# Performance work log

Hardware: AMD Instinct MI355X
Metric: run time of the kernel (lower is better)

## Reference

```python
import jax, jax.numpy as jnp
import numpy as np

N, T, DM = 8192, 32, 128   # nodes, patches, d_model (d_in = T*DM = 4096)
M, NNZ = 1024, 131072      # hyperedges, incidences
EPS = 1e-5
SLOPE = 0.2


def _bn(x, g, b, axes):
    # BatchNorm with batch statistics (training-mode math, eval dropout)
    m = jnp.mean(x, axis=axes, keepdims=True)
    v = jnp.var(x, axis=axes, keepdims=True)
    return (x - m) / jnp.sqrt(v + EPS) * g + b


def _hconv(x, he_attr, he_n, he_e, W, att, bias, heads):
    # PyG HypergraphConv, use_attention=True, attention_mode='node', concat=False
    out = W.shape[1] // heads
    xt = (x @ W).reshape(N, heads, out)          # [N, H, F]
    et = (he_attr @ W).reshape(M, heads, out)    # [M, H, F]
    xi = xt[he_n]                                # [nnz, H, F] gather node feats
    ej = et[he_e]                                # [nnz, H, F] gather edge feats
    alpha = jnp.sum(jnp.concatenate([xi, ej], axis=-1) * att, axis=-1)  # [nnz, H]
    alpha = jax.nn.leaky_relu(alpha, SLOPE)
    # segment softmax grouped by hyperedge (attention_mode='node')
    amax = jax.ops.segment_max(alpha, he_e, num_segments=M)
    ex = jnp.exp(alpha - amax[he_e])
    alpha = ex / jax.ops.segment_sum(ex, he_e, num_segments=M)[he_e]
    # degree normalizers (hyperedge_weight == 1)
    ones = jnp.ones((NNZ,), x.dtype)
    Dn = jax.ops.segment_sum(ones, he_n, num_segments=N)
    Dinv = jnp.where(Dn > 0, 1.0 / Dn, 0.0)
    Bm = jax.ops.segment_sum(ones, he_e, num_segments=M)
    Binv = jnp.where(Bm > 0, 1.0 / Bm, 0.0)
    # node -> edge, then edge -> node message passing
    eo = jax.ops.segment_sum(alpha[:, :, None] * Binv[he_e][:, None, None] * xi,
                             he_e, num_segments=M)                     # [M, H, F]
    no = jax.ops.segment_sum(alpha[:, :, None] * Dinv[he_n][:, None, None] * eo[he_e],
                             he_n, num_segments=N)                     # [N, H, F]
    return no.mean(axis=1) + bias  # concat=False -> mean over heads


def setup_inputs() -> dict:
    key = jax.random.key(0)
    ks = jax.random.split(key, 16)
    d_in = T * DM
    s = 0.02
    inp = {
        "x": jax.random.normal(ks[0], (N, T, DM), jnp.float32),
        "he_nodes": jax.random.randint(ks[1], (NNZ,), 0, N),
        "he_edges": jax.random.randint(ks[2], (NNZ,), 0, M),
        "W1": jax.random.normal(ks[3], (d_in, DM), jnp.float32) * s,
        "b1": jnp.zeros((DM,), jnp.float32),
        "g1": jnp.ones((DM,), jnp.float32), "be1": jnp.zeros((DM,), jnp.float32),
        "Wh1": jax.random.normal(ks[4], (DM, 4 * DM), jnp.float32) * s,
        "att1": jax.random.normal(ks[5], (1, 4, 2 * DM), jnp.float32) * s,
        "bh1": jnp.zeros((DM,), jnp.float32),
        "g2": jnp.ones((DM,), jnp.float32), "be2": jnp.zeros((DM,), jnp.float32),
        "Wh2": jax.random.normal(ks[6], (DM, DM), jnp.float32) * s,
        "att2": jax.random.normal(ks[7], (1, 1, 2 * DM), jnp.float32) * s,
        "bh2": jnp.zeros((DM,), jnp.float32),
        "g3": jnp.ones((DM,), jnp.float32), "be3": jnp.zeros((DM,), jnp.float32),
        "W3": jax.random.normal(ks[8], (DM, d_in), jnp.float32) * s,
        "b3": jnp.zeros((d_in,), jnp.float32),
        "g4": jnp.ones((DM,), jnp.float32), "be4": jnp.zeros((DM,), jnp.float32),
    }
    return inp


def reference(x, he_nodes, he_edges, W1, b1, g1, be1, Wh1, att1, bh1,
              g2, be2, Wh2, att2, bh2, g3, be3, W3, b3, g4, be4):
    src = x
    h = x.reshape(N, T * DM)
    h = jax.nn.leaky_relu(h @ W1 + b1, SLOPE)
    h = _bn(h, g1, be1, 0)
    # hyperedge_attr = incidence^T @ h  (== to_dense_adj(...).T @ h)
    he_attr = jax.ops.segment_sum(h[he_nodes], he_edges, num_segments=M)
    h = h + _hconv(h, he_attr, he_nodes, he_edges, Wh1, att1, bh1, 4)
    h = _bn(h, g2, be2, 0)
    he_attr = jax.ops.segment_sum(h[he_nodes], he_edges, num_segments=M)
    h = h + _hconv(h, he_attr, he_nodes, he_edges, Wh2, att2, bh2, 1)
    h = _bn(h, g3, be3, 0)
    h = jax.nn.leaky_relu(h @ W3 + b3, SLOPE)
    h = src + h.reshape(N, T, DM)
    h = _bn(h, g4, be4, (0, 1))  # BN over channel DM, stats over (N, T)
    return h
```

## Files before the change

### kernel.cpp

```cpp
#include <hip/hip_runtime.h>
#include <hip/hip_bf16.h>
#include <math.h>

#define NN   8192
#define TT   32
#define DIN  4096
#define MME  1024
#define NNZK 131072
#define EPSV 1e-5f
#define MALL (NN + MME)

typedef __attribute__((ext_vector_type(8))) short bf16x8;
typedef __attribute__((ext_vector_type(4))) float f32x4;

__device__ __forceinline__ float lrelu(float v){ return v > 0.f ? v : 0.2f*v; }
__device__ __forceinline__ short f2b(float f){
    union { __hip_bfloat16 h; short s; } u; u.h = __float2bfloat16(f); return u.s;
}
__device__ __forceinline__ float b2f(short s){
    union { float f; unsigned u; } u; u.u = ((unsigned)(unsigned short)s) << 16; return u.f;
}

__global__ void zero_i(int* p, int n){ int i = blockIdx.x*256 + threadIdx.x; if (i < n) p[i] = 0; }
__global__ void zero_f(float* p, int n){ int i = blockIdx.x*256 + threadIdx.x; if (i < n) p[i] = 0.f; }
__global__ void copy_i(const int* a, int* b, int n){ int i = blockIdx.x*256 + threadIdx.x; if (i < n) b[i] = a[i]; }

__global__ void count_seg(const int* __restrict__ he_n, const int* __restrict__ he_e,
                          int* __restrict__ ncnt, int* __restrict__ ecnt){
    int k = blockIdx.x*256 + threadIdx.x;
    if (k < NNZK){ atomicAdd(&ecnt[he_e[k]], 1); atomicAdd(&ncnt[he_n[k]], 1); }
}

__global__ void scan_excl(const int* __restrict__ cnt, int* __restrict__ off, int n){
    __shared__ int buf[1024];
    __shared__ int carry;
    int t = threadIdx.x;
    if (t == 0) carry = 0;
    __syncthreads();
    for (int base = 0; base < n; base += 1024){
        int i = base + t;
        int v = (i < n) ? cnt[i] : 0;
        buf[t] = v; __syncthreads();
        for (int s = 1; s < 1024; s <<= 1){
            int tmp = (t >= s) ? buf[t - s] : 0;
            __syncthreads();
            buf[t] += tmp;
            __syncthreads();
        }
        if (i < n) off[i] = carry + buf[t] - v;
        __syncthreads();
        if (t == 1023) carry += buf[1023];
        __syncthreads();
    }
    if (t == 0) off[n] = carry;
}

__global__ void fill_perm(const int* __restrict__ seg, int* __restrict__ cur, int* __restrict__ perm){
    int k = blockIdx.x*256 + threadIdx.x;
    if (k < NNZK){ int p = atomicAdd(&cur[seg[k]], 1); perm[p] = k; }
}

__global__ void wconv_t(const float* __restrict__ W, __hip_bfloat16* __restrict__ BT, int K, int N){
    __shared__ float tile[32][33];
    int k0 = blockIdx.y*32, n0 = blockIdx.x*32;
    int tx = threadIdx.x & 31, ty = threadIdx.x >> 5;
    for (int i = ty; i < 32; i += 8) tile[i][tx] = W[(size_t)(k0+i)*N + n0+tx];
    __syncthreads();
    for (int i = ty; i < 32; i += 8)
        BT[(size_t)(n0+i)*K + k0 + tx] = __float2bfloat16(tile[tx][i]);
}

#define SWZ(b) ((b) ^ ((((b) >> 6) & 7) << 4))

template<int MODE>
__global__ __launch_bounds__(256) void gemm_nt(
    const float* __restrict__ Aact, const __hip_bfloat16* __restrict__ Bwt,
    float* __restrict__ C, __hip_bfloat16* __restrict__ Cb, const float* __restrict__ bias,
    int M, int N, int K, int kchunk)
{
    __shared__ f32x4 WsRaw[512];
    __shared__ f32x4 XsRaw[512];
    char* Ws = (char*)WsRaw;
    char* Xs = (char*)XsRaw;
    const int tid = threadIdx.x;
    const int lane = tid & 63;
    const int w = tid >> 6;
    const int m0 = blockIdx.y << 7, n0 = blockIdx.x << 7;
    const int kz = blockIdx.z * kchunk;
    const int wN = (w >> 1) << 6, wM = (w & 1) << 6;

    const int s0 = tid, s1 = tid + 256;
    const int r0 = s0 >> 2, k0b = (s0 & 3) << 3;
    const int r1 = s1 >> 2, k1b = (s1 & 3) << 3;
    const float* pX0 = Aact + (size_t)(m0 + r0)*K + kz + k0b;
    const float* pX1 = Aact + (size_t)(m0 + r1)*K + kz + k1b;
    const __hip_bfloat16* pW0 = Bwt + (size_t)(n0 + r0)*K + kz + k0b;
    const __hip_bfloat16* pW1 = Bwt + (size_t)(n0 + r1)*K + kz + k1b;
    const int wo0 = SWZ(s0 << 4), wo1 = SWZ(s1 << 4);

    int rwOff[4], rxOff[4];
#pragma unroll
    for (int f = 0; f < 4; f++){
        rwOff[f] = SWZ((wN + f*16 + (lane & 15))*64 + ((lane >> 4) << 4));
        rxOff[f] = SWZ((wM + f*16 + (lane & 15))*64 + ((lane >> 4) << 4));
    }

    f32x4 acc[4][4] = {};

    float4 x0l = *(const float4*)pX0, x0h = *(const float4*)(pX0+4);
    float4 x1l = *(const float4*)pX1, x1h = *(const float4*)(pX1+4);
    bf16x8 w0 = *(const bf16x8*)pW0, w1 = *(const bf16x8*)pW1;

    const int nsteps = kchunk >> 5;
    for (int ks = 0; ks < nsteps; ks++){
        bf16x8 vx0, vx1;
        vx0[0]=f2b(x0l.x); vx0[1]=f2b(x0l.y); vx0[2]=f2b(x0l.z); vx0[3]=f2b(x0l.w);
        vx0[4]=f2b(x0h.x); vx0[5]=f2b(x0h.y); vx0[6]=f2b(x0h.z); vx0[7]=f2b(x0h.w);
        vx1[0]=f2b(x1l.x); vx1[1]=f2b(x1l.y); vx1[2]=f2b(x1l.z); vx1[3]=f2b(x1l.w);
        vx1[4]=f2b(x1h.x); vx1[5]=f2b(x1h.y); vx1[6]=f2b(x1h.z); vx1[7]=f2b(x1h.w);
        __syncthreads();
        *(bf16x8*)(Xs + wo0) = vx0;
        *(bf16x8*)(Xs + wo1) = vx1;
        *(bf16x8*)(Ws + wo0) = w0;
        *(bf16x8*)(Ws + wo1) = w1;
        __syncthreads();
        if (ks + 1 < nsteps){
            pX0 += 32; pX1 += 32; pW0 += 32; pW1 += 32;
            x0l = *(const float4*)pX0; x0h = *(const float4*)(pX0+4);
            x1l = *(const float4*)pX1; x1h = *(const float4*)(pX1+4);
            w0 = *(const bf16x8*)pW0;  w1 = *(const bf16x8*)pW1;
        }
        bf16x8 wf[4], xf[4];
#pragma unroll
        for (int f = 0; f < 4; f++){
            wf[f] = *(const bf16x8*)(Ws + rwOff[f]);
            xf[f] = *(const bf16x8*)(Xs + rxOff[f]);
        }
#pragma unroll
        for (int i = 0; i < 4; i++)
#pragma unroll
            for (int j = 0; j < 4; j++)
                acc[i][j] = __builtin_amdgcn_mfma_f32_16x16x32_bf16(wf[i], xf[j], acc[i][j], 0, 0, 0);
    }

    const int mc = wM + (lane & 15);
    const int ncb = wN + ((lane >> 4) << 2);
#pragma unroll
    for (int j = 0; j < 4; j++){
        int row = m0 + mc + j*16;
#pragma unroll
        for (int i = 0; i < 4; i++){
            int col = n0 + ncb + i*16;
            f32x4 v = acc[i][j];
            if (MODE == 0){
                *(float4*)&C[(size_t)row*N + col] = *(float4*)&v;
            } else if (MODE == 2){
                __hip_bfloat16* Cz = Cb + (size_t)blockIdx.z * ((size_t)M * (size_t)N);
                short4 sv = { f2b(v[0]), f2b(v[1]), f2b(v[2]), f2b(v[3]) };
                *(short4*)&Cz[(size_t)row*N + col] = sv;
            } else {
                float4 b4 = *(const float4*)&bias[col];
                short4 sv = { f2b(lrelu(v[0] + b4.x)), f2b(lrelu(v[1] + b4.y)),
                              f2b(lrelu(v[2] + b4.z)), f2b(lrelu(v[3] + b4.w)) };
                *(short4*)&Cb[(size_t)row*N + col] = sv;
            }
        }
    }
}

__global__ void reduce8s(const __hip_bfloat16* __restrict__ part, const float* __restrict__ bias,
                         float* __restrict__ out, int nf4, int parts, float* __restrict__ slots){
    int tid = threadIdx.x;
    int i = blockIdx.x*256 + tid;
    const short4* p4 = (const short4*)part;
    short4 v0 = p4[i];
    float4 s = { b2f(v0.x), b2f(v0.y), b2f(v0.z), b2f(v0.w) };
    for (int z = 1; z < parts; z++){
        short4 p = p4[(size_t)z*nf4 + i];
        s.x += b2f(p.x); s.y += b2f(p.y); s.z += b2f(p.z); s.w += b2f(p.w);
    }
    int c0 = (i & 31) << 2;
    s.x = lrelu(s.x + bias[c0+0]); s.y = lrelu(s.y + bias[c0+1]);
    s.z = lrelu(s.z + bias[c0+2]); s.w = lrelu(s.w + bias[c0+3]);
    ((float4*)out)[i] = s;
    __shared__ float S[128], Q[128];
    if (tid < 128){ S[tid] = 0.f; Q[tid] = 0.f; }
    __syncthreads();
    atomicAdd(&S[c0+0], s.x); atomicAdd(&Q[c0+0], s.x*s.x);
    atomicAdd(&S[c0+1], s.y); atomicAdd(&Q[c0+1], s.y*s.y);
    atomicAdd(&S[c0+2], s.z); atomicAdd(&Q[c0+2], s.z*s.z);
    atomicAdd(&S[c0+3], s.w); atomicAdd(&Q[c0+3], s.w*s.w);
    __syncthreads();
    if (tid < 128){
        int slot = blockIdx.x & 31;
        atomicAdd(&slots[slot*256 + tid], S[tid]);
        atomicAdd(&slots[slot*256 + 128 + tid], Q[tid]);
    }
}

__global__ __launch_bounds__(256) void final_stats(
    const float4* __restrict__ x, const short4* __restrict__ f,
    float* __restrict__ slots, int n4)
{
    int tid = threadIdx.x;
    float4 s = {0,0,0,0}, q = {0,0,0,0};
    int stride = gridDim.x*256;
    for (int i = blockIdx.x*256 + tid; i < n4; i += stride){
        float4 xv = x[i]; short4 fv = f[i];
        float y0 = xv.x + b2f(fv.x), y1 = xv.y + b2f(fv.y);
        float y2 = xv.z + b2f(fv.z), y3 = xv.w + b2f(fv.w);
        s.x += y0; q.x += y0*y0;
        s.y += y1; q.y += y1*y1;
        s.z += y2; q.z += y2*y2;
        s.w += y3; q.w += y3*y3;
    }
    __shared__ float S[128], Q[128];
    if (tid < 128){ S[tid] = 0.f; Q[tid] = 0.f; }
    __syncthreads();
    int c0 = (tid & 31) << 2;
    atomicAdd(&S[c0+0], s.x); atomicAdd(&Q[c0+0], q.x);
    atomicAdd(&S[c0+1], s.y); atomicAdd(&Q[c0+1], q.y);
    atomicAdd(&S[c0+2], s.z); atomicAdd(&Q[c0+2], q.z);
    atomicAdd(&S[c0+3], s.w); atomicAdd(&Q[c0+3], q.w);
    __syncthreads();
    if (tid < 128){
        int slot = blockIdx.x & 31;
        atomicAdd(&slots[slot*256 + tid], S[tid]);
        atomicAdd(&slots[slot*256 + 128 + tid], Q[tid]);
    }
}

__global__ __launch_bounds__(256) void final_apply(
    const float4* __restrict__ x, const short4* __restrict__ f,
    const float* __restrict__ coef, float4* __restrict__ out, int n4)
{
    int tid = threadIdx.x;
    int c0 = (tid & 31) << 2;
    float4 sc = *(const float4*)&coef[c0];
    float4 sh = *(const float4*)&coef[128 + c0];
    int stride = gridDim.x*256;
    for (int i = blockIdx.x*256 + tid; i < n4; i += stride){
        float4 xv = x[i]; short4 fv = f[i];
        float4 v;
        v.x = (xv.x + b2f(fv.x))*sc.x + sh.x;
        v.y = (xv.y + b2f(fv.y))*sc.y + sh.y;
        v.z = (xv.z + b2f(fv.z))*sc.z + sh.z;
        v.w = (xv.w + b2f(fv.w))*sc.w + sh.w;
        out[i] = v;
    }
}

__global__ void bn_stats_v2(const float* __restrict__ x, float* __restrict__ slots, int rows){
    int cg = threadIdx.x & 31, rg = threadIdx.x >> 5;
    float4 s = {0,0,0,0}, q = {0,0,0,0};
    for (int r = blockIdx.x*8 + rg; r < rows; r += gridDim.x*8){
        float4 v = ((const float4*)x)[(size_t)r*32 + cg];
        s.x += v.x; q.x += v.x*v.x;
        s.y += v.y; q.y += v.y*v.y;
        s.z += v.z; q.z += v.z*v.z;
        s.w += v.w; q.w += v.w*v.w;
    }
    __shared__ float S[128], Q[128];
    if (threadIdx.x < 128){ S[threadIdx.x] = 0.f; Q[threadIdx.x] = 0.f; }
    __syncthreads();
    int c0 = cg << 2;
    atomicAdd(&S[c0+0], s.x); atomicAdd(&Q[c0+0], q.x);
    atomicAdd(&S[c0+1], s.y); atomicAdd(&Q[c0+1], q.y);
    atomicAdd(&S[c0+2], s.z); atomicAdd(&Q[c0+2], q.z);
    atomicAdd(&S[c0+3], s.w); atomicAdd(&Q[c0+3], q.w);
    __syncthreads();
    if (threadIdx.x < 128){
        int slot = blockIdx.x & 31;
        atomicAdd(&slots[slot*256 + threadIdx.x], S[threadIdx.x]);
        atomicAdd(&slots[slot*256 + 128 + threadIdx.x], Q[threadIdx.x]);
    }
}

__global__ void bn_finalize2(const float* __restrict__ slots, int nslots,
                             const float* __restrict__ g, const float* __restrict__ b,
                             float invR, float* __restrict__ coef){
    int c = threadIdx.x;
    float s = 0.f, q = 0.f;
    for (int k = 0; k < nslots; k++){ s += slots[k*256 + c]; q += slots[k*256 + 128 + c]; }
    float m = s*invR;
    float v = q*invR - m*m;
    float sc = g[c]*rsqrtf(v + EPSV);
    coef[c] = sc;
    coef[128 + c] = b[c] - m*sc;
}

__global__ void bn_apply4(float4* __restrict__ x, const float* __restrict__ coef, size_t n4){
    size_t i = (size_t)blockIdx.x*blockDim.x + threadIdx.x;
    size_t stride = (size_t)gridDim.x*blockDim.x;
    for (; i < n4; i += stride){
        int c0 = (int)(i & 31) * 4;
        float4 v = x[i];
        v.x = v.x*coef[c0+0] + coef[128+c0+0];
        v.y = v.y*coef[c0+1] + coef[128+c0+1];
        v.z = v.z*coef[c0+2] + coef[128+c0+2];
        v.w = v.w*coef[c0+3] + coef[128+c0+3];
        x[i] = v;
    }
}

__global__ void seg_sum_edge(const int* __restrict__ eoff, const int* __restrict__ eperm,
                             const int* __restrict__ he_n, const float* __restrict__ h,
                             float* __restrict__ out){
    int m = blockIdx.x, c = threadIdx.x;
    int s0 = eoff[m], cnt = eoff[m+1] - s0;
    __shared__ int sn[128];
    float acc = 0.f;
    for (int base = 0; base < cnt; base += 128){
        int i = base + c;
        if (i < cnt) sn[c] = he_n[eperm[s0+i]];
        __syncthreads();
        int lim = min(128, cnt - base);
        for (int j = 0; j < lim; j++) acc += h[(size_t)sn[j]*128 + c];
        __syncthreads();
    }
    out[(size_t)m*128 + c] = acc;
}

template<int H>
__global__ void row_att(const float* __restrict__ xt, const float* __restrict__ att,
                        int aoff, float* __restrict__ out){
    int n = blockIdx.x, lane = threadIdx.x;
#pragma unroll
    for (int h = 0; h < H; h++){
        const float* xr = xt + (size_t)n*(H*128) + h*128;
        const float* ar = att + h*256 + aoff;
        float s = xr[lane]*ar[lane] + xr[lane+64]*ar[lane+64];
        for (int d = 32; d > 0; d >>= 1) s += __shfl_down(s, d);
        if (lane == 0) out[n*H + h] = s;
    }
}

template<int H>
__global__ void seg_softmax(const int* __restrict__ eoff, const int* __restrict__ eperm,
                            const int* __restrict__ he_n,
                            const float* __restrict__ ax, const float* __restrict__ ae,
                            float* __restrict__ alpha){
    int m = blockIdx.x, t = threadIdx.x;
    int s0 = eoff[m], cnt = eoff[m+1] - s0;
    if (cnt == 0) return;
    __shared__ float red[128];
    float aeh[H];
#pragma unroll
    for (int h = 0; h < H; h++) aeh[h] = ae[m*H + h];
    float lmax[H];
#pragma unroll
    for (int h = 0; h < H; h++) lmax[h] = -1e30f;
    for (int i = t; i < cnt; i += 128){
        int k = eperm[s0+i]; int n = he_n[k];
#pragma unroll
        for (int h = 0; h < H; h++){
            float v = lrelu(ax[n*H + h] + aeh[h]);
            alpha[(size_t)k*H + h] = v;
            lmax[h] = fmaxf(lmax[h], v);
        }
    }
    float gmax[H];
#pragma unroll
    for (int h = 0; h < H; h++){
        red[t] = lmax[h]; __syncthreads();
        for (int s = 64; s > 0; s >>= 1){ if (t < s) red[t] = fmaxf(red[t], red[t+s]); __syncthreads(); }
        gmax[h] = red[0]; __syncthreads();
    }
    float lsum[H];
#pragma unroll
    for (int h = 0; h < H; h++) lsum[h] = 0.f;
    for (int i = t; i < cnt; i += 128){
        int k = eperm[s0+i];
#pragma unroll
        for (int h = 0; h < H; h++){
            float ex = __expf(alpha[(size_t)k*H + h] - gmax[h]);
            alpha[(size_t)k*H + h] = ex;
            lsum[h] += ex;
        }
    }
    float ginv[H];
#pragma unroll
    for (int h = 0; h < H; h++){
        red[t] = lsum[h]; __syncthreads();
        for (int s = 64; s > 0; s >>= 1){ if (t < s) red[t] += red[t+s]; __syncthreads(); }
        ginv[h] = 1.f/red[0]; __syncthreads();
    }
    for (int i = t; i < cnt; i += 128){
        int k = eperm[s0+i];
#pragma unroll
        for (int h = 0; h < H; h++) alpha[(size_t)k*H + h] *= ginv[h];
    }
}

__global__ void seg_eo4(const int* __restrict__ eoff, const int* __restrict__ eperm,
                        const int* __restrict__ he_n,
                        const float* __restrict__ alpha, const float* __restrict__ xt,
                        float* __restrict__ eo){
    int m = blockIdx.x;
    int c = threadIdx.x & 127, hb = threadIdx.x >> 7;
    int s0 = eoff[m], cnt = eoff[m+1] - s0;
    __shared__ int sn[128];
    __shared__ float sa[128][4];
    float acc0 = 0.f, acc1 = 0.f;
    for (int base = 0; base < cnt; base += 128){
        int i = base + threadIdx.x;
        if (threadIdx.x < 128 && i < cnt){
            int k = eperm[s0+i];
            sn[threadIdx.x] = he_n[k];
#pragma unroll
            for (int h = 0; h < 4; h++) sa[threadIdx.x][h] = alpha[(size_t)k*4 + h];
        }
        __syncthreads();
        int lim = min(128, cnt - base);
        for (int j = 0; j < lim; j++){
            const float* xr = xt + (size_t)sn[j]*512;
            acc0 += sa[j][hb]   * xr[hb*128 + c];
            acc1 += sa[j][hb+2] * xr[(hb+2)*128 + c];
        }
        __syncthreads();
    }
    float binv = cnt > 0 ? 1.f/(float)cnt : 0.f;
    eo[(size_t)m*512 + hb*128 + c]     = acc0*binv;
    eo[(size_t)m*512 + (hb+2)*128 + c] = acc1*binv;
}

__global__ void seg_eo1(const int* __restrict__ eoff, const int* __restrict__ eperm,
                        const int* __restrict__ he_n,
                        const float* __restrict__ alpha, const float* __restrict__ xt,
                        float* __restrict__ eo){
    int m = blockIdx.x, c = threadIdx.x;
    int s0 = eoff[m], cnt = eoff[m+1] - s0;
    __shared__ int sn[128];
    __shared__ float sa[128];
    float acc = 0.f;
    for (int base = 0; base < cnt; base += 128){
        int i = base + c;
        if (i < cnt){
            int k = eperm[s0+i];
            sn[c] = he_n[k];
            sa[c] = alpha[k];
        }
        __syncthreads();
        int lim = min(128, cnt - base);
        for (int j = 0; j < lim; j++) acc += sa[j]*xt[(size_t)sn[j]*128 + c];
        __syncthreads();
    }
    float binv = cnt > 0 ? 1.f/(float)cnt : 0.f;
    eo[(size_t)m*128 + c] = acc*binv;
}

template<int H>
__global__ void seg_node_out(const int* __restrict__ noff, const int* __restrict__ nperm,
                             const int* __restrict__ he_e,
                             const float* __restrict__ alpha, const float* __restrict__ eo,
                             const float* __restrict__ hin, const float* __restrict__ bias,
                             float* __restrict__ hout){
    int n = blockIdx.x, c = threadIdx.x;
    int s0 = noff[n], cnt = noff[n+1] - s0;
    float acc = 0.f;
    for (int i = 0; i < cnt; i++){
        int k = nperm[s0+i]; int e = he_e[k];
        const float* er = eo + (size_t)e*(128*H);
#pragma unroll
        for (int h = 0; h < H; h++) acc += alpha[(size_t)k*H + h]*er[h*128 + c];
    }
    float dinv = cnt > 0 ? 1.f/((float)cnt*(float)H) : 0.f;
    hout[(size_t)n*128 + c] = hin[(size_t)n*128 + c] + bias[c] + acc*dinv;
}

extern "C" void kernel_launch(void* const* d_in, const int* in_sizes, int n_in,
                              void* d_out, int out_size, void* d_ws, size_t ws_size,
                              hipStream_t stream){
    const float* x    = (const float*)d_in[0];
    const int*   he_n = (const int*)  d_in[1];
    const int*   he_e = (const int*)  d_in[2];
    const float* W1   = (const float*)d_in[3];
    const float* b1   = (const float*)d_in[4];
    const float* g1   = (const float*)d_in[5];
    const float* be1  = (const float*)d_in[6];
    const float* Wh1  = (const float*)d_in[7];
    const float* att1 = (const float*)d_in[8];
    const float* bh1  = (const float*)d_in[9];
    const float* g2   = (const float*)d_in[10];
    const float* be2  = (const float*)d_in[11];
    const float* Wh2  = (const float*)d_in[12];
    const float* att2 = (const float*)d_in[13];
    const float* bh2  = (const float*)d_in[14];
    const float* g3   = (const float*)d_in[15];
    const float* be3  = (const float*)d_in[16];
    const float* W3   = (const float*)d_in[17];
    const float* b3   = (const float*)d_in[18];
    const float* g4   = (const float*)d_in[19];
    const float* be4  = (const float*)d_in[20];
    float* out = (float*)d_out;

    char* ws = (char*)d_ws;
    size_t off = 0;
    auto alloc = [&](size_t bytes)->char*{ char* p = ws + off; off += (bytes + 255) & ~(size_t)255; return p; };

    char* big = alloc((size_t)NN*DIN*2);
    __hip_bfloat16* fbuf = (__hip_bfloat16*)big;
    __hip_bfloat16* part = (__hip_bfloat16*)big;
    float*          xt1  = (float*)(big + (size_t)16*NN*128*2);

    float* hall1  = (float*)alloc((size_t)MALL*128*4);
    float* hall2  = (float*)alloc((size_t)MALL*128*4);
    float* h3     = (float*)alloc((size_t)NN*128*4);
    float* xt2    = (float*)alloc((size_t)MALL*128*4);
    float* eo     = (float*)alloc((size_t)MME*512*4);
    float* alpha  = (float*)alloc((size_t)NNZK*4*4);
    float* ax     = (float*)alloc((size_t)NN*4*4);
    float* ae     = (float*)alloc((size_t)MME*4*4);
    float* slots  = (float*)alloc((size_t)32*256*4);
    float* coef   = (float*)alloc(256*4);
    __hip_bfloat16* W1T  = (__hip_bfloat16*)alloc((size_t)128*DIN*2);
    __hip_bfloat16* Wh1T = (__hip_bfloat16*)alloc((size_t)512*128*2);
    __hip_bfloat16* Wh2T = (__hip_bfloat16*)alloc((size_t)128*128*2);
    __hip_bfloat16* W3T  = (__hip_bfloat16*)alloc((size_t)DIN*128*2);
    int* ecnt  = (int*)alloc(MME*4);
    int* ncnt  = (int*)alloc(NN*4);
    int* eoffb = (int*)alloc((MME+1)*4);
    int* ecur  = (int*)alloc(MME*4);
    int* noffb = (int*)alloc((NN+1)*4);
    int* ncur  = (int*)alloc(NN*4);
    int* eperm = (int*)alloc((size_t)NNZK*4);
    int* nperm = (int*)alloc((size_t)NNZK*4);

    zero_i<<<(MME+NN+255)/256, 256, 0, stream>>>(ecnt, MME+NN);
    count_seg<<<NNZK/256, 256, 0, stream>>>(he_n, he_e, ncnt, ecnt);
    scan_excl<<<1, 1024, 0, stream>>>(ecnt, eoffb, MME);
    scan_excl<<<1, 1024, 0, stream>>>(ncnt, noffb, NN);
    copy_i<<<(MME+255)/256, 256, 0, stream>>>(eoffb, ecur, MME);
    copy_i<<<(NN+255)/256, 256, 0, stream>>>(noffb, ncur, NN);
    fill_perm<<<NNZK/256, 256, 0, stream>>>(he_e, ecur, eperm);
    fill_perm<<<NNZK/256, 256, 0, stream>>>(he_n, ncur, nperm);

    wconv_t<<<dim3(128/32, DIN/32), 256, 0, stream>>>(W1,  W1T,  DIN, 128);
    wconv_t<<<dim3(512/32, 128/32), 256, 0, stream>>>(Wh1, Wh1T, 128, 512);
    wconv_t<<<dim3(128/32, 128/32), 256, 0, stream>>>(Wh2, Wh2T, 128, 128);
    wconv_t<<<dim3(DIN/32, 128/32), 256, 0, stream>>>(W3,  W3T,  128, DIN);

    gemm_nt<2><<<dim3(1, NN/128, 16), 256, 0, stream>>>(x, W1T, nullptr, part, nullptr, NN, 128, DIN, DIN/16);
    zero_f<<<32, 256, 0, stream>>>(slots, 32*256);
    reduce8s<<<NN*128/4/256, 256, 0, stream>>>(part, b1, hall1, NN*128/4, 16, slots);
    bn_finalize2<<<1, 128, 0, stream>>>(slots, 32, g1, be1, 1.f/NN, coef);
    bn_apply4<<<1024, 256, 0, stream>>>((float4*)hall1, coef, (size_t)NN*32);

    seg_sum_edge<<<MME, 128, 0, stream>>>(eoffb, eperm, he_n, hall1, hall1 + (size_t)NN*128);
    gemm_nt<0><<<dim3(512/128, MALL/128, 1), 256, 0, stream>>>(hall1, Wh1T, xt1, nullptr, nullptr, MALL, 512, 128, 128);
    row_att<4><<<NN, 64, 0, stream>>>(xt1, att1, 0, ax);
    row_att<4><<<MME, 64, 0, stream>>>(xt1 + (size_t)NN*512, att1, 128, ae);
    seg_softmax<4><<<MME, 128, 0, stream>>>(eoffb, eperm, he_n, ax, ae, alpha);
    seg_eo4<<<MME, 256, 0, stream>>>(eoffb, eperm, he_n, alpha, xt1, eo);
    seg_node_out<4><<<NN, 128, 0, stream>>>(noffb, nperm, he_e, alpha, eo, hall1, bh1, hall2);
    zero_f<<<32, 256, 0, stream>>>(slots, 32*256);
    bn_stats_v2<<<256, 256, 0, stream>>>(hall2, slots, NN);
    bn_finalize2<<<1, 128, 0, stream>>>(slots, 32, g2, be2, 1.f/NN, coef);
    bn_apply4<<<1024, 256, 0, stream>>>((float4*)hall2, coef, (size_t)NN*32);

    seg_sum_edge<<<MME, 128, 0, stream>>>(eoffb, eperm, he_n, hall2, hall2 + (size_t)NN*128);
    gemm_nt<0><<<dim3(1, MALL/128, 1), 256, 0, stream>>>(hall2, Wh2T, xt2, nullptr, nullptr, MALL, 128, 128, 128);
    row_att<1><<<NN, 64, 0, stream>>>(xt2, att2, 0, ax);
    row_att<1><<<MME, 64, 0, stream>>>(xt2 + (size_t)NN*128, att2, 128, ae);
    seg_softmax<1><<<MME, 128, 0, stream>>>(eoffb, eperm, he_n, ax, ae, alpha);
    seg_eo1<<<MME, 128, 0, stream>>>(eoffb, eperm, he_n, alpha, xt2, eo);
    seg_node_out<1><<<NN, 128, 0, stream>>>(noffb, nperm, he_e, alpha, eo, hall2, bh2, h3);
    zero_f<<<32, 256, 0, stream>>>(slots, 32*256);
    bn_stats_v2<<<256, 256, 0, stream>>>(h3, slots, NN);
    bn_finalize2<<<1, 128, 0, stream>>>(slots, 32, g3, be3, 1.f/NN, coef);
    bn_apply4<<<1024, 256, 0, stream>>>((float4*)h3, coef, (size_t)NN*32);

    gemm_nt<3><<<dim3(DIN/128, NN/128, 1), 256, 0, stream>>>(h3, W3T, nullptr, fbuf, b3, NN, DIN, 128, 128);
    zero_f<<<32, 256, 0, stream>>>(slots, 32*256);
    final_stats<<<2048, 256, 0, stream>>>((const float4*)x, (const short4*)fbuf, slots, NN*TT*32);
    bn_finalize2<<<1, 128, 0, stream>>>(slots, 32, g4, be4, 1.f/((float)NN*TT), coef);
    final_apply<<<2048, 256, 0, stream>>>((const float4*)x, (const short4*)fbuf, coef, (float4*)out, NN*TT*32);
}
```

Before: 562.8 us.

## Cache bf16 copy of input during first GEMM and reuse it for final residual BN

The first GEMM now writes the bf16-converted input tile to a side buffer as it streams x. The final stats and apply kernels read this bf16 copy instead of the fp32 input, halving residual read traffic in two passes over the 128 MiB tensor, at the cost of an extra 64 MiB write and bf16 rounding of the residual path. The serial single-block prefix scan is also replaced with a per-thread chunked scan using wave shuffles.

Measured after the change: 574.6 us. 1.02x slower.

```diff
diff --git a/kernel.cpp b/kernel.cpp
--- a/kernel.cpp
+++ b/kernel.cpp
@@ -32,27 +32,36 @@
 }
 
 __global__ void scan_excl(const int* __restrict__ cnt, int* __restrict__ off, int n){
-    __shared__ int buf[1024];
-    __shared__ int carry;
     int t = threadIdx.x;
-    if (t == 0) carry = 0;
-    __syncthreads();
-    for (int base = 0; base < n; base += 1024){
-        int i = base + t;
-        int v = (i < n) ? cnt[i] : 0;
-        buf[t] = v; __syncthreads();
-        for (int s = 1; s < 1024; s <<= 1){
-            int tmp = (t >= s) ? buf[t - s] : 0;
-            __syncthreads();
-            buf[t] += tmp;
-            __syncthreads();
-        }
-        if (i < n) off[i] = carry + buf[t] - v;
-        __syncthreads();
-        if (t == 1023) carry += buf[1023];
-        __syncthreads();
-    }
-    if (t == 0) off[n] = carry;
+    int lane = t & 63, wv = t >> 6;
+    int chunk = n >> 10;
+    int base = t*chunk;
+    int s = 0;
+#pragma unroll 4
+    for (int i = 0; i < chunk; i++) s += cnt[base+i];
+    int v = s;
+    for (int d = 1; d < 64; d <<= 1){
+        int u = __shfl_up(v, d);
+        if (lane >= d) v += u;
+    }
+    __shared__ int wsum[16];
+    if (lane == 63) wsum[wv] = v;
+    __syncthreads();
+    if (wv == 0 && lane < 16){
+        int w2 = wsum[lane];
+        for (int d = 1; d < 16; d <<= 1){
+            int u = __shfl_up(w2, d);
+            if (lane >= d) w2 += u;
+        }
+        wsum[lane] = w2;
+    }
+    __syncthreads();
+    int excl = v - s + (wv > 0 ? wsum[wv-1] : 0);
+    for (int i = 0; i < chunk; i++){
+        off[base+i] = excl;
+        excl += cnt[base+i];
+    }
+    if (t == 1023) off[n] = excl;
 }
 
 __global__ void fill_perm(const int* __restrict__ seg, int* __restrict__ cur, int* __restrict__ perm){
@@ -76,7 +85,7 @@
 __global__ __launch_bounds__(256) void gemm_nt(
     const float* __restrict__ Aact, const __hip_bfloat16* __restrict__ Bwt,
     float* __restrict__ C, __hip_bfloat16* __restrict__ Cb, const float* __restrict__ bias,
-    int M, int N, int K, int kchunk)
+    __hip_bfloat16* __restrict__ xb, int M, int N, int K, int kchunk)
 {
     __shared__ f32x4 WsRaw[512];
     __shared__ f32x4 XsRaw[512];
@@ -96,6 +105,8 @@
     const float* pX1 = Aact + (size_t)(m0 + r1)*K + kz + k1b;
     const __hip_bfloat16* pW0 = Bwt + (size_t)(n0 + r0)*K + kz + k0b;
     const __hip_bfloat16* pW1 = Bwt + (size_t)(n0 + r1)*K + kz + k1b;
+    __hip_bfloat16* pXB0 = xb + (size_t)(m0 + r0)*K + kz + k0b;
+    __hip_bfloat16* pXB1 = xb + (size_t)(m0 + r1)*K + kz + k1b;
     const int wo0 = SWZ(s0 << 4), wo1 = SWZ(s1 << 4);
 
     int rwOff[4], rxOff[4];
@@ -118,6 +129,10 @@
         vx0[4]=f2b(x0h.x); vx0[5]=f2b(x0h.y); vx0[6]=f2b(x0h.z); vx0[7]=f2b(x0h.w);
         vx1[0]=f2b(x1l.x); vx1[1]=f2b(x1l.y); vx1[2]=f2b(x1l.z); vx1[3]=f2b(x1l.w);
         vx1[4]=f2b(x1h.x); vx1[5]=f2b(x1h.y); vx1[6]=f2b(x1h.z); vx1[7]=f2b(x1h.w);
+        if (MODE == 4){
+            *(bf16x8*)(pXB0 + ks*32) = vx0;
+            *(bf16x8*)(pXB1 + ks*32) = vx1;
+        }
         __syncthreads();
         *(bf16x8*)(Xs + wo0) = vx0;
         *(bf16x8*)(Xs + wo1) = vx1;
@@ -154,7 +169,7 @@
             f32x4 v = acc[i][j];
             if (MODE == 0){
                 *(float4*)&C[(size_t)row*N + col] = *(float4*)&v;
-            } else if (MODE == 2){
+            } else if (MODE == 4){
                 __hip_bfloat16* Cz = Cb + (size_t)blockIdx.z * ((size_t)M * (size_t)N);
                 short4 sv = { f2b(v[0]), f2b(v[1]), f2b(v[2]), f2b(v[3]) };
                 *(short4*)&Cz[(size_t)row*N + col] = sv;
@@ -199,29 +214,29 @@
 }
 
 __global__ __launch_bounds__(256) void final_stats(
-    const float4* __restrict__ x, const short4* __restrict__ f,
-    float* __restrict__ slots, int n4)
+    const bf16x8* __restrict__ xb, const bf16x8* __restrict__ f,
+    float* __restrict__ slots, int n8)
 {
     int tid = threadIdx.x;
-    float4 s = {0,0,0,0}, q = {0,0,0,0};
+    float s[8] = {0,0,0,0,0,0,0,0}, q[8] = {0,0,0,0,0,0,0,0};
     int stride = gridDim.x*256;
-    for (int i = blockIdx.x*256 + tid; i < n4; i += stride){
-        float4 xv = x[i]; short4 fv = f[i];
-        float y0 = xv.x + b2f(fv.x), y1 = xv.y + b2f(fv.y);
-        float y2 = xv.z + b2f(fv.z), y3 = xv.w + b2f(fv.w);
-        s.x += y0; q.x += y0*y0;
-        s.y += y1; q.y += y1*y1;
-        s.z += y2; q.z += y2*y2;
-        s.w += y3; q.w += y3*y3;
+    for (int i = blockIdx.x*256 + tid; i < n8; i += stride){
+        bf16x8 xv = xb[i], fv = f[i];
+#pragma unroll
+        for (int j = 0; j < 8; j++){
+            float y = b2f(xv[j]) + b2f(fv[j]);
+            s[j] += y; q[j] += y*y;
+        }
     }
     __shared__ float S[128], Q[128];
     if (tid < 128){ S[tid] = 0.f; Q[tid] = 0.f; }
     __syncthreads();
-    int c0 = (tid & 31) << 2;
-    atomicAdd(&S[c0+0], s.x); atomicAdd(&Q[c0+0], q.x);
-    atomicAdd(&S[c0+1], s.y); atomicAdd(&Q[c0+1], q.y);
-    atomicAdd(&S[c0+2], s.z); atomicAdd(&Q[c0+2], q.z);
-    atomicAdd(&S[c0+3], s.w); atomicAdd(&Q[c0+3], q.w);
+    int c0 = (tid & 15) << 3;
+#pragma unroll
+    for (int j = 0; j < 8; j++){
+        atomicAdd(&S[c0+j], s[j]);
+        atomicAdd(&Q[c0+j], q[j]);
+    }
     __syncthreads();
     if (tid < 128){
         int slot = blockIdx.x & 31;
@@ -231,22 +246,28 @@
 }
 
 __global__ __launch_bounds__(256) void final_apply(
-    const float4* __restrict__ x, const short4* __restrict__ f,
-    const float* __restrict__ coef, float4* __restrict__ out, int n4)
+    const bf16x8* __restrict__ xb, const bf16x8* __restrict__ f,
+    const float* __restrict__ coef, float4* __restrict__ out, int n8)
 {
     int tid = threadIdx.x;
-    int c0 = (tid & 31) << 2;
-    float4 sc = *(const float4*)&coef[c0];
-    float4 sh = *(const float4*)&coef[128 + c0];
+    int c0 = (tid & 15) << 3;
+    float sc[8], sh[8];
+#pragma unroll
+    for (int j = 0; j < 8; j++){ sc[j] = coef[c0+j]; sh[j] = coef[128+c0+j]; }
     int stride = gridDim.x*256;
-    for (int i = blockIdx.x*256 + tid; i < n4; i += stride){
-        float4 xv = x[i]; short4 fv = f[i];
-        float4 v;
-        v.x = (xv.x + b2f(fv.x))*sc.x + sh.x;
-        v.y = (xv.y + b2f(fv.y))*sc.y + sh.y;
-        v.z = (xv.z + b2f(fv.z))*sc.z + sh.z;
-        v.w = (xv.w + b2f(fv.w))*sc.w + sh.w;
-        out[i] = v;
+    for (int i = blockIdx.x*256 + tid; i < n8; i += stride){
+        bf16x8 xv = xb[i], fv = f[i];
+        float4 lo, hi;
+        lo.x = (b2f(xv[0]) + b2f(fv[0]))*sc[0] + sh[0];
+        lo.y = (b2f(xv[1]) + b2f(fv[1]))*sc[1] + sh[1];
+        lo.z = (b2f(xv[2]) + b2f(fv[2]))*sc[2] + sh[2];
+        lo.w = (b2f(xv[3]) + b2f(fv[3]))*sc[3] + sh[3];
+        hi.x = (b2f(xv[4]) + b2f(fv[4]))*sc[4] + sh[4];
+        hi.y = (b2f(xv[5]) + b2f(fv[5]))*sc[5] + sh[5];
+        hi.z = (b2f(xv[6]) + b2f(fv[6]))*sc[6] + sh[6];
+        hi.w = (b2f(xv[7]) + b2f(fv[7]))*sc[7] + sh[7];
+        out[2*i]   = lo;
+        out[2*i+1] = hi;
     }
 }
 
@@ -502,6 +523,7 @@
     __hip_bfloat16* fbuf = (__hip_bfloat16*)big;
     __hip_bfloat16* part = (__hip_bfloat16*)big;
     float*          xt1  = (float*)(big + (size_t)16*NN*128*2);
+    __hip_bfloat16* xbuf = (__hip_bfloat16*)alloc((size_t)NN*DIN*2);
 
     float* hall1  = (float*)alloc((size_t)MALL*128*4);
     float* hall2  = (float*)alloc((size_t)MALL*128*4);
@@ -540,14 +562,14 @@
     wconv_t<<<dim3(128/32, 128/32), 256, 0, stream>>>(Wh2, Wh2T, 128, 128);
     wconv_t<<<dim3(DIN/32, 128/32), 256, 0, stream>>>(W3,  W3T,  128, DIN);
 
-    gemm_nt<2><<<dim3(1, NN/128, 16), 256, 0, stream>>>(x, W1T, nullptr, part, nullptr, NN, 128, DIN, DIN/16);
+    gemm_nt<4><<<dim3(1, NN/128, 16), 256, 0, stream>>>(x, W1T, nullptr, part, nullptr, xbuf, NN, 128, DIN, DIN/16);
     zero_f<<<32, 256, 0, stream>>>(slots, 32*256);
     reduce8s<<<NN*128/4/256, 256, 0, stream>>>(part, b1, hall1, NN*128/4, 16, slots);
     bn_finalize2<<<1, 128, 0, stream>>>(slots, 32, g1, be1, 1.f/NN, coef);
     bn_apply4<<<1024, 256, 0, stream>>>((float4*)hall1, coef, (size_t)NN*32);
 
     seg_sum_edge<<<MME, 128, 0, stream>>>(eoffb, eperm, he_n, hall1, hall1 + (size_t)NN*128);
-    gemm_nt<0><<<dim3(512/128, MALL/128, 1), 256, 0, stream>>>(hall1, Wh1T, xt1, nullptr, nullptr, MALL, 512, 128, 128);
+    gemm_nt<0><<<dim3(512/128, MALL/128, 1), 256, 0, stream>>>(hall1, Wh1T, xt1, nullptr, nullptr, nullptr, MALL, 512, 128, 128);
     row_att<4><<<NN, 64, 0, stream>>>(xt1, att1, 0, ax);
     row_att<4><<<MME, 64, 0, stream>>>(xt1 + (size_t)NN*512, att1, 128, ae);
     seg_softmax<4><<<MME, 128, 0, stream>>>(eoffb, eperm, he_n, ax, ae, alpha);
@@ -559,7 +581,7 @@
     bn_apply4<<<1024, 256, 0, stream>>>((float4*)hall2, coef, (size_t)NN*32);
 
     seg_sum_edge<<<MME, 128, 0, stream>>>(eoffb, eperm, he_n, hall2, hall2 + (size_t)NN*128);
-    gemm_nt<0><<<dim3(1, MALL/128, 1), 256, 0, stream>>>(hall2, Wh2T, xt2, nullptr, nullptr, MALL, 128, 128, 128);
+    gemm_nt<0><<<dim3(1, MALL/128, 1), 256, 0, stream>>>(hall2, Wh2T, xt2, nullptr, nullptr, nullptr, MALL, 128, 128, 128);
     row_att<1><<<NN, 64, 0, stream>>>(xt2, att2, 0, ax);
     row_att<1><<<MME, 64, 0, stream>>>(xt2 + (size_t)NN*128, att2, 128, ae);
     seg_softmax<1><<<MME, 128, 0, stream>>>(eoffb, eperm, he_n, ax, ae, alpha);
@@ -570,9 +592,9 @@
     bn_finalize2<<<1, 128, 0, stream>>>(slots, 32, g3, be3, 1.f/NN, coef);
     bn_apply4<<<1024, 256, 0, stream>>>((float4*)h3, coef, (size_t)NN*32);
 
-    gemm_nt<3><<<dim3(DIN/128, NN/128, 1), 256, 0, stream>>>(h3, W3T, nullptr, fbuf, b3, NN, DIN, 128, 128);
+    gemm_nt<3><<<dim3(DIN/128, NN/128, 1), 256, 0, stream>>>(h3, W3T, nullptr, fbuf, b3, nullptr, NN, DIN, 128, 128);
     zero_f<<<32, 256, 0, stream>>>(slots, 32*256);
-    final_stats<<<2048, 256, 0, stream>>>((const float4*)x, (const short4*)fbuf, slots, NN*TT*32);
+    final_stats<<<2048, 256, 0, stream>>>((const bf16x8*)xbuf, (const bf16x8*)fbuf, slots, NN*DIN/8);
     bn_finalize2<<<1, 128, 0, stream>>>(slots, 32, g4, be4, 1.f/((float)NN*TT), coef);
-    final_apply<<<2048, 256, 0, stream>>>((const float4*)x, (const short4*)fbuf, coef, (float4*)out, NN*TT*32);
-}
+    final_apply<<<2048, 256, 0, stream>>>((const bf16x8*)xbuf, (const bf16x8*)fbuf, coef, (float4*)out, NN*DIN/8);
+}
```
